# Kernel tuning notes

Hardware: AMD Instinct MI355X
Metric: run time of the kernel (lower is better)

## Reference

```python
import jax, jax.numpy as jnp
import numpy as np

EPSILON = 1e-05
LOG_2PI = float(np.log(2.0 * np.pi))


def setup_inputs() -> dict:
    key = jax.random.key(0)
    k1, k2, k3 = jax.random.split(key, 3)
    B, S, K, N = 64, 1000, 12, 80  # batch, seq, n_states, n_channels
    x = jax.random.normal(k1, (B, S, N), dtype=jnp.float32)
    mu = jax.random.normal(k2, (B, K, N), dtype=jnp.float32)
    # Positive-definite covariances per (batch, state)
    A = jax.random.normal(k3, (B, K, N, N), dtype=jnp.float32)
    sigma = A @ jnp.swapaxes(A, -1, -2) / N + jnp.eye(N, dtype=jnp.float32)
    return {"x": x, "mu": mu, "sigma": sigma}


def reference(x, mu, sigma):
    """Batched-over-states MVN log-likelihood.

    x: (B, S, N); mu: (B, K, N); sigma: (B, K, N, N).
    Returns log_likelihood: (B, S, K).
    """
    N = x.shape[-1]
    # add_epsilon with diag=True: epsilon * I on the diagonal
    sigma = sigma + jnp.asarray(EPSILON, sigma.dtype) * jnp.eye(N, dtype=sigma.dtype)
    L = jnp.linalg.cholesky(sigma)  # (B, K, N, N), batched across states
    diff = x[:, :, None, :] - mu[:, None, :, :]  # (B, S, K, N)
    # Solve L z = diff, batched: L -> (B, 1, K, N, N), diff -> (B, S, K, N, 1)
    z = jax.scipy.linalg.solve_triangular(L[:, None], diff[..., None], lower=True)[..., 0]
    quad = jnp.sum(z * z, axis=-1)  # (B, S, K)
    logdet_half = jnp.sum(jnp.log(jnp.diagonal(L, axis1=-2, axis2=-1)), axis=-1)  # (B, K)
    ll = -0.5 * quad - logdet_half[:, None, :] - 0.5 * N * jnp.asarray(LOG_2PI, x.dtype)
    return ll  # (B, S, K)
```

## Files before the change

kernel.cpp:

```cpp
#include <hip/hip_runtime.h>

#define Bb 64
#define Ss 1000
#define Kk 12
#define Nn 80
#define CTERM 73.51508265637381f
#define STA 84

typedef __attribute__((ext_vector_type(8))) short short8;
typedef __attribute__((ext_vector_type(4))) float f32x4;

static __device__ __forceinline__ unsigned short f2bf(float f) {
    unsigned u = __builtin_bit_cast(unsigned, f);
    unsigned r = u + 0x7FFFu + ((u >> 16) & 1u);
    return (unsigned short)(r >> 16);
}
static __device__ __forceinline__ float bf2f(unsigned short h) {
    unsigned u = ((unsigned)h) << 16;
    return __builtin_bit_cast(float, u);
}

__global__ __launch_bounds__(256, 3) void prep_kernel(
    const float* __restrict__ sigma, const float* __restrict__ mu,
    const float* __restrict__ x,
    uint4* __restrict__ wsWh, uint4* __restrict__ wsWl,
    float* __restrict__ wsV, float* __restrict__ wsL,
    uint4* __restrict__ Xh, uint4* __restrict__ Xl, int doX)
{
    __shared__ float Ls[Nn * STA];
    __shared__ float LT[Nn * Nn];
    __shared__ float invd[Nn];
    __shared__ float mus[Nn];
    __shared__ float ldp[4];

    const int bk  = blockIdx.x;
    const int tid = threadIdx.x;
    const int w   = tid >> 6;
    const int l   = tid & 63;
    const int r2  = l + 64;

    const float4* sp4 = (const float4*)(sigma + (size_t)bk * Nn * Nn);
    #pragma unroll
    for (int it = 0; it < 7; ++it) {
        int ci = tid + 256 * it;
        if (ci < 1600) {
            float4 v = sp4[ci];
            int r = ci / 20, c4 = 4 * (ci - 20 * r);
            *(float4*)&Ls[r * STA + c4] = v;
        }
    }
    if (tid < Nn) mus[tid] = mu[(size_t)bk * Nn + tid];
    __syncthreads();
    if (tid < Nn) Ls[tid * STA + tid] += 1e-5f;
    __syncthreads();

    float ldacc = 0.0f;
    for (int p = 0; p < 20; ++p) {
        const int j0 = 4 * p;
        const bool a1 = (l >= j0);
        const bool a2 = (l < 16) && (r2 >= j0);

        if (w == (p & 3)) {
            float B00 = Ls[j0*STA+j0];
            float B10 = Ls[(j0+1)*STA+j0], B11 = Ls[(j0+1)*STA+j0+1];
            float B20 = Ls[(j0+2)*STA+j0], B21 = Ls[(j0+2)*STA+j0+1], B22 = Ls[(j0+2)*STA+j0+2];
            float B30 = Ls[(j0+3)*STA+j0], B31 = Ls[(j0+3)*STA+j0+1], B32 = Ls[(j0+3)*STA+j0+2], B33 = Ls[(j0+3)*STA+j0+3];
            float rv0 = rsqrtf(B00);
            float l10 = B10*rv0, l20 = B20*rv0, l30 = B30*rv0;
            float t11 = fmaf(-l10,l10,B11);                    float rv1 = rsqrtf(t11);
            float l21 = fmaf(-l20,l10,B21)*rv1;
            float l31 = fmaf(-l30,l10,B31)*rv1;
            float t22 = fmaf(-l21,l21,fmaf(-l20,l20,B22));     float rv2 = rsqrtf(t22);
            float l32 = fmaf(-l31,l21,fmaf(-l30,l20,B32))*rv2;
            float t33 = fmaf(-l32,l32,fmaf(-l31,l31,fmaf(-l30,l30,B33)));
            float rv3 = rsqrtf(t33);
            ldacc += 0.5f * (logf(B00) + logf(t11) + logf(t22) + logf(t33));
            if (l == 0) { invd[j0]=rv0; invd[j0+1]=rv1; invd[j0+2]=rv2; invd[j0+3]=rv3; }

            float b0=0.f,b1=0.f,b2=0.f,b3=0.f, c0=0.f,c1=0.f,c2=0.f,c3=0.f;
            if (a1) {
                float4 a = *(float4*)&Ls[l * STA + j0];
                b0 = a.x * rv0;
                b1 = fmaf(-l10, b0, a.y) * rv1;
                b2 = fmaf(-l21, b1, fmaf(-l20, b0, a.z)) * rv2;
                b3 = fmaf(-l32, b2, fmaf(-l31, b1, fmaf(-l30, b0, a.w))) * rv3;
                *(float4*)&Ls[l * STA + j0] = make_float4(b0, b1, b2, b3);
            }
            if (a2) {
                float4 a = *(float4*)&Ls[r2 * STA + j0];
                c0 = a.x * rv0;
                c1 = fmaf(-l10, c0, a.y) * rv1;
                c2 = fmaf(-l21, c1, fmaf(-l20, c0, a.z)) * rv2;
                c3 = fmaf(-l32, c2, fmaf(-l31, c1, fmaf(-l30, c0, a.w))) * rv3;
                *(float4*)&Ls[r2 * STA + j0] = make_float4(c0, c1, c2, c3);
            }
            LT[ j0   *Nn + l] = (l  > j0  ) ? b0 : 0.f;
            LT[(j0+1)*Nn + l] = (l  > j0+1) ? b1 : 0.f;
            LT[(j0+2)*Nn + l] = (l  > j0+2) ? b2 : 0.f;
            LT[(j0+3)*Nn + l] = (l  > j0+3) ? b3 : 0.f;
            if (l < 16) {
                LT[ j0   *Nn + r2] = (r2 > j0  ) ? c0 : 0.f;
                LT[(j0+1)*Nn + r2] = (r2 > j0+1) ? c1 : 0.f;
                LT[(j0+2)*Nn + r2] = (r2 > j0+2) ? c2 : 0.f;
                LT[(j0+3)*Nn + r2] = (r2 > j0+3) ? c3 : 0.f;
            }
        }
        __syncthreads();

        float4 bv = make_float4(0.f,0.f,0.f,0.f), cv = make_float4(0.f,0.f,0.f,0.f);
        if (a1) bv = *(float4*)&Ls[l * STA + j0];
        if (a2) cv = *(float4*)&Ls[r2 * STA + j0];
        const int gs0 = p + 1;
        const int g0 = gs0 + ((w - gs0) & 3);
        #pragma unroll 2
        for (int g = g0; g < 20; g += 4) {
            float4 u0 = *(const float4*)&LT[ j0   *Nn + 4*g];
            float4 u1 = *(const float4*)&LT[(j0+1)*Nn + 4*g];
            float4 u2 = *(const float4*)&LT[(j0+2)*Nn + 4*g];
            float4 u3 = *(const float4*)&LT[(j0+3)*Nn + 4*g];
            if (a1) {
                float4 t = *(float4*)&Ls[l * STA + 4*g];
                t.x = fmaf(-bv.x,u0.x, fmaf(-bv.y,u1.x, fmaf(-bv.z,u2.x, fmaf(-bv.w,u3.x, t.x))));
                t.y = fmaf(-bv.x,u0.y, fmaf(-bv.y,u1.y, fmaf(-bv.z,u2.y, fmaf(-bv.w,u3.y, t.y))));
                t.z = fmaf(-bv.x,u0.z, fmaf(-bv.y,u1.z, fmaf(-bv.z,u2.z, fmaf(-bv.w,u3.z, t.z))));
                t.w = fmaf(-bv.x,u0.w, fmaf(-bv.y,u1.w, fmaf(-bv.z,u2.w, fmaf(-bv.w,u3.w, t.w))));
                *(float4*)&Ls[l * STA + 4*g] = t;
            }
            if (a2) {
                float4 t = *(float4*)&Ls[r2 * STA + 4*g];
                t.x = fmaf(-cv.x,u0.x, fmaf(-cv.y,u1.x, fmaf(-cv.z,u2.x, fmaf(-cv.w,u3.x, t.x))));
                t.y = fmaf(-cv.x,u0.y, fmaf(-cv.y,u1.y, fmaf(-cv.z,u2.y, fmaf(-cv.w,u3.y, t.y))));
                t.z = fmaf(-cv.x,u0.z, fmaf(-cv.y,u1.z, fmaf(-cv.z,u2.z, fmaf(-cv.w,u3.z, t.z))));
                t.w = fmaf(-cv.x,u0.w, fmaf(-cv.y,u1.w, fmaf(-cv.z,u2.w, fmaf(-cv.w,u3.w, t.w))));
                *(float4*)&Ls[r2 * STA + 4*g] = t;
            }
        }
    }
    if (l == 0) ldp[w] = ldacc;
    __syncthreads();
    if (tid == 0) wsL[bk] = ldp[0] + ldp[1] + ldp[2] + ldp[3];

    if (tid < Nn) {
        #pragma unroll
        for (int g = 0; g < 20; ++g)
            *(float4*)&Ls[tid * STA + 4*g] = make_float4(0.f, 0.f, 0.f, 0.f);
        Ls[tid * STA + tid] = 1.0f;
    }
    __syncthreads();

    for (int p = 0; p < 20; ++p) {
        const int i0 = 4 * p;
        const bool b1a = (i0 + 3 >= l);
        const bool b2a = (l < 16) && (i0 + 3 >= r2);

        if (w == (p & 3)) {
            float m10 = LT[ i0   *Nn + i0+1];
            float m20 = LT[ i0   *Nn + i0+2];
            float m30 = LT[ i0   *Nn + i0+3];
            float m21 = LT[(i0+1)*Nn + i0+2];
            float m31 = LT[(i0+1)*Nn + i0+3];
            float m32 = LT[(i0+2)*Nn + i0+3];
            float4 iv = *(const float4*)&invd[i0];
            if (b1a) {
                float4 a = *(float4*)&Ls[l * STA + i0];
                float w0 = a.x * iv.x;
                float w1 = fmaf(-w0, m10, a.y) * iv.y;
                float w2 = fmaf(-w1, m21, fmaf(-w0, m20, a.z)) * iv.z;
                float w3 = fmaf(-w2, m32, fmaf(-w1, m31, fmaf(-w0, m30, a.w))) * iv.w;
                *(float4*)&Ls[l * STA + i0] = make_float4(w0, w1, w2, w3);
            }
            if (b2a) {
                float4 a = *(float4*)&Ls[r2 * STA + i0];
                float v0 = a.x * iv.x;
                float v1 = fmaf(-v0, m10, a.y) * iv.y;
                float v2 = fmaf(-v1, m21, fmaf(-v0, m20, a.z)) * iv.z;
                float v3 = fmaf(-v2, m32, fmaf(-v1, m31, fmaf(-v0, m30, a.w))) * iv.w;
                *(float4*)&Ls[r2 * STA + i0] = make_float4(v0, v1, v2, v3);
            }
        }
        __syncthreads();

        float4 wv = make_float4(0.f,0.f,0.f,0.f), vv = make_float4(0.f,0.f,0.f,0.f);
        if (b1a) wv = *(float4*)&Ls[l * STA + i0];
        if (b2a) vv = *(float4*)&Ls[r2 * STA + i0];
        if (b1a | b2a) {
            const int gs0 = p + 1;
            const int g0 = gs0 + ((w - gs0) & 3);
            #pragma unroll 2
            for (int g = g0; g < 20; g += 4) {
                float4 u0 = *(const float4*)&LT[ i0   *Nn + 4*g];
                float4 u1 = *(const float4*)&LT[(i0+1)*Nn + 4*g];
                float4 u2 = *(const float4*)&LT[(i0+2)*Nn + 4*g];
                float4 u3 = *(const float4*)&LT[(i0+3)*Nn + 4*g];
                if (b1a) {
                    float4 t = *(float4*)&Ls[l * STA + 4*g];
                    t.x = fmaf(-wv.x,u0.x, fmaf(-wv.y,u1.x, fmaf(-wv.z,u2.x, fmaf(-wv.w,u3.x, t.x))));
                    t.y = fmaf(-wv.x,u0.y, fmaf(-wv.y,u1.y, fmaf(-wv.z,u2.y, fmaf(-wv.w,u3.y, t.y))));
                    t.z = fmaf(-wv.x,u0.z, fmaf(-wv.y,u1.z, fmaf(-wv.z,u2.z, fmaf(-wv.w,u3.z, t.z))));
                    t.w = fmaf(-wv.x,u0.w, fmaf(-wv.y,u1.w, fmaf(-wv.z,u2.w, fmaf(-wv.w,u3.w, t.w))));
                    *(float4*)&Ls[l * STA + 4*g] = t;
                }
                if (b2a) {
                    float4 t = *(float4*)&Ls[r2 * STA + 4*g];
                    t.x = fmaf(-vv.x,u0.x, fmaf(-vv.y,u1.x, fmaf(-vv.z,u2.x, fmaf(-vv.w,u3.x, t.x))));
                    t.y = fmaf(-vv.x,u0.y, fmaf(-vv.y,u1.y, fmaf(-vv.z,u2.y, fmaf(-vv.w,u3.y, t.y))));
                    t.z = fmaf(-vv.x,u0.z, fmaf(-vv.y,u1.z, fmaf(-vv.z,u2.z, fmaf(-vv.w,u3.z, t.z))));
                    t.w = fmaf(-vv.x,u0.w, fmaf(-vv.y,u1.w, fmaf(-vv.z,u2.w, fmaf(-vv.w,u3.w, t.w))));
                    *(float4*)&Ls[r2 * STA + 4*g] = t;
                }
            }
        }
    }
    __syncthreads();

    {
        float* vpart = LT;
        float s1 = 0.f, s2 = 0.f;
        const int c0 = 20 * w;
        #pragma unroll 4
        for (int cc = 0; cc < 20; ++cc) {
            int c = c0 + cc;
            float mc = mus[c];
            s1 = fmaf(Ls[c * STA + l], mc, s1);
            if (l < 16) s2 = fmaf(Ls[c * STA + r2], mc, s2);
        }
        vpart[w * Nn + l] = s1;
        if (l < 16) vpart[w * Nn + r2] = s2;
        __syncthreads();
        if (tid < Nn)
            wsV[(size_t)bk * Nn + tid] =
                vpart[tid] + vpart[Nn + tid] + vpart[2*Nn + tid] + vpart[3*Nn + tid];
    }
    const int n = l & 15, quad = l >> 4;
    uint4* ph = wsWh + (size_t)bk * 800;
    uint4* pq = wsWl + (size_t)bk * 800;
    for (int f = w; f < 10; f += 4) {
        int ks = f / 5, mt = f - 5 * ks;
        int m = 16 * mt + n, kb = 32 * ks + 8 * quad;
        unsigned hh[8], lo[8];
        #pragma unroll
        for (int j = 0; j < 8; ++j) {
            float wj = Ls[(kb + j) * STA + m];
            unsigned short h = f2bf(wj);
            hh[j] = h; lo[j] = f2bf(wj - bf2f(h));
        }
        ph[f*64 + l] = make_uint4(hh[0]|(hh[1]<<16), hh[2]|(hh[3]<<16), hh[4]|(hh[5]<<16), hh[6]|(hh[7]<<16));
        pq[f*64 + l] = make_uint4(lo[0]|(lo[1]<<16), lo[2]|(lo[3]<<16), lo[4]|(lo[5]<<16), lo[6]|(lo[7]<<16));
    }
    for (int mt = w; mt < 5; mt += 4) {
        if (quad < 2) {
            int m = 16 * mt + n, kb = 64 + 8 * quad;
            unsigned hh[8], lo[8];
            #pragma unroll
            for (int j = 0; j < 8; ++j) {
                float wj = Ls[(kb + j) * STA + m];
                unsigned short h = f2bf(wj);
                hh[j] = h; lo[j] = f2bf(wj - bf2f(h));
            }
            ph[640 + mt*32 + l] = make_uint4(hh[0]|(hh[1]<<16), hh[2]|(hh[3]<<16), hh[4]|(hh[5]<<16), hh[6]|(hh[7]<<16));
            pq[640 + mt*32 + l] = make_uint4(lo[0]|(lo[1]<<16), lo[2]|(lo[3]<<16), lo[4]|(lo[5]<<16), lo[6]|(lo[7]<<16));
        }
    }

    if (doX) {
        const int wid = bk * 4 + w;
        const int qd = l >> 4, n2 = l & 15;
        #pragma unroll
        for (int it = 0; it < 4; ++it) {
            int G = wid + 3072 * it;
            if (G >= 12096) break;
            int b2  = G / 189;
            int rem = G - b2 * 189;
            int sg  = rem / 3, ks = rem - 3 * sg;
            int s   = sg * 16 + n2;
            int k0  = 32 * ks + 8 * qd;
            float d[8] = {0.f,0.f,0.f,0.f,0.f,0.f,0.f,0.f};
            if (s < Ss) {
                const float* xp = x + ((size_t)b2 * Ss + s) * Nn + k0;
                float4 f0 = *(const float4*)xp;
                float4 f1 = *(const float4*)(xp + 4);
                d[0]=f0.x; d[1]=f0.y; d[2]=f0.z; d[3]=f0.w;
                d[4]=f1.x; d[5]=f1.y; d[6]=f1.z; d[7]=f1.w;
            }
            unsigned hh[8], lo[8];
            #pragma unroll
            for (int j = 0; j < 8; ++j) {
                unsigned short h = f2bf(d[j]);
                hh[j] = h; lo[j] = f2bf(d[j] - bf2f(h));
            }
            size_t slot = ((size_t)(b2 * 64 + sg) * 3 + ks) * 64 + l;
            Xh[slot] = make_uint4(hh[0]|(hh[1]<<16), hh[2]|(hh[3]<<16), hh[4]|(hh[5]<<16), hh[6]|(hh[7]<<16));
            Xl[slot] = make_uint4(lo[0]|(lo[1]<<16), lo[2]|(lo[3]<<16), lo[4]|(lo[5]<<16), lo[6]|(lo[7]<<16));
        }
    }
}

__global__ __launch_bounds__(256) void ll_kernel2(
    const uint4* __restrict__ Xh, const uint4* __restrict__ Xl,
    const uint4* __restrict__ wsWh, const uint4* __restrict__ wsWl,
    const float* __restrict__ wsV, const float* __restrict__ wsL,
    float* __restrict__ out)
{
    __shared__ uint4 WhL[960], WlL[960];
    const int b = blockIdx.x;
    const int k = blockIdx.y;
    const int bk = b * Kk + k;
    const int tid = threadIdx.x;
    const int wv = tid >> 6, lane = tid & 63;
    const int n = lane & 15, quad = lane >> 4;

    const uint4* gh = wsWh + (size_t)bk * 800;
    const uint4* gl = wsWl + (size_t)bk * 800;
    #pragma unroll
    for (int it = 0; it < 3; ++it) {
        int i = tid + 256 * it;
        if (i < 640) { WhL[i] = gh[i]; WlL[i] = gl[i]; }
    }
    #pragma unroll
    for (int it = 0; it < 2; ++it) {
        int i = tid + 256 * it;
        if (i < 320) {
            int mt = i >> 6, ln = i & 63, qd = (ln >> 4);
            uint4 vh = make_uint4(0,0,0,0), vl = make_uint4(0,0,0,0);
            if (qd < 2) { vh = gh[640 + mt*32 + ln]; vl = gl[640 + mt*32 + ln]; }
            WhL[640 + i] = vh; WlL[640 + i] = vl;
        }
    }
    __syncthreads();

    const float ld = wsL[bk];
    f32x4 vf[5];
    #pragma unroll
    for (int mt = 0; mt < 5; ++mt)
        vf[mt] = *(const f32x4*)&wsV[(size_t)bk * Nn + 16*mt + 4*quad];

    for (int st = 0; st < 8; ++st) {
        const int sg0 = st * 8 + wv * 2;
        short8 bh[2][3], bl[2][3];
        #pragma unroll
        for (int t = 0; t < 2; ++t)
            #pragma unroll
            for (int ks = 0; ks < 3; ++ks) {
                size_t base = ((size_t)(b * 64 + sg0 + t) * 3 + ks) * 64 + lane;
                bh[t][ks] = __builtin_bit_cast(short8, Xh[base]);
                bl[t][ks] = __builtin_bit_cast(short8, Xl[base]);
            }

        f32x4 acc[2][5];
        #pragma unroll
        for (int t = 0; t < 2; ++t)
            #pragma unroll
            for (int mt = 0; mt < 5; ++mt) acc[t][mt] = (f32x4){0.f,0.f,0.f,0.f};

        #pragma unroll
        for (int ks = 0; ks < 3; ++ks) {
            #pragma unroll
            for (int mt = 0; mt < 5; ++mt) {
                const int fi = (ks < 2) ? (ks*5 + mt)*64 + lane : 640 + mt*64 + lane;
                short8 wh = __builtin_bit_cast(short8, WhL[fi]);
                short8 wl = __builtin_bit_cast(short8, WlL[fi]);
                #pragma unroll
                for (int t = 0; t < 2; ++t) {
                    acc[t][mt] = __builtin_amdgcn_mfma_f32_16x16x32_bf16(wh, bh[t][ks], acc[t][mt], 0, 0, 0);
                    acc[t][mt] = __builtin_amdgcn_mfma_f32_16x16x32_bf16(wl, bh[t][ks], acc[t][mt], 0, 0, 0);
                    acc[t][mt] = __builtin_amdgcn_mfma_f32_16x16x32_bf16(wh, bl[t][ks], acc[t][mt], 0, 0, 0);
                }
            }
        }

        #pragma unroll
        for (int t = 0; t < 2; ++t) {
            float q2 = 0.f;
            #pragma unroll
            for (int mt = 0; mt < 5; ++mt)
                #pragma unroll
                for (int r = 0; r < 4; ++r) {
                    float y = acc[t][mt][r] - vf[mt][r];
                    q2 = fmaf(y, y, q2);
                }
            q2 += __shfl_xor(q2, 16, 64);
            q2 += __shfl_xor(q2, 32, 64);
            int gs = st * 128 + wv * 32 + 16 * t + n;
            if (lane < 16 && gs < Ss)
                out[((size_t)b * Ss + gs) * Kk + k] = -0.5f * q2 - ld - CTERM;
        }
    }
}

__global__ __launch_bounds__(256) void ll_kernel(
    const float* __restrict__ x,
    const uint4* __restrict__ wsWh, const uint4* __restrict__ wsWl,
    const float* __restrict__ wsV, const float* __restrict__ wsL,
    float* __restrict__ out)
{
    const int b    = blockIdx.x;
    const int st   = blockIdx.y;
    const int tid  = threadIdx.x;
    const int wv   = tid >> 6, lane = tid & 63;
    const int n    = lane & 15, quad = lane >> 4;
    const int sbase = st * 128 + wv * 32;

    short8 xh[2][3], xl[2][3];
    #pragma unroll
    for (int t = 0; t < 2; ++t) {
        int gs = sbase + 16 * t + n;
        #pragma unroll
        for (int ks = 0; ks < 3; ++ks) {
            int kb = 32 * ks + 8 * quad;
            float d[8] = {0.f,0.f,0.f,0.f,0.f,0.f,0.f,0.f};
            if (gs < Ss && kb < Nn) {
                const float* xp = x + ((size_t)b * Ss + gs) * Nn + kb;
                float4 f0 = *(const float4*)xp;
                float4 f1 = *(const float4*)(xp + 4);
                d[0]=f0.x; d[1]=f0.y; d[2]=f0.z; d[3]=f0.w;
                d[4]=f1.x; d[5]=f1.y; d[6]=f1.z; d[7]=f1.w;
            }
            short8 h, lo2;
            #pragma unroll
            for (int j = 0; j < 8; ++j) {
                unsigned short hv = f2bf(d[j]);
                h[j]   = (short)hv;
                lo2[j] = (short)f2bf(d[j] - bf2f(hv));
            }
            xh[t][ks] = h; xl[t][ks] = lo2;
        }
    }

    for (int k = 0; k < Kk; ++k) {
        const int bk = b * Kk + k;
        const uint4* ah_p = wsWh + (size_t)bk * 800;
        const uint4* al_p = wsWl + (size_t)bk * 800;

        f32x4 acc[2][5];
        #pragma unroll
        for (int t = 0; t < 2; ++t)
            #pragma unroll
            for (int mt = 0; mt < 5; ++mt) acc[t][mt] = (f32x4){0.f,0.f,0.f,0.f};

        #pragma unroll
        for (int ks = 0; ks < 3; ++ks) {
            short8 ah[5], al[5];
            if (ks < 2) {
                #pragma unroll
                for (int mt = 0; mt < 5; ++mt) {
                    ah[mt] = __builtin_bit_cast(short8, ah_p[(ks*5 + mt)*64 + lane]);
                    al[mt] = __builtin_bit_cast(short8, al_p[(ks*5 + mt)*64 + lane]);
                }
            } else {
                #pragma unroll
                for (int mt = 0; mt < 5; ++mt) {
                    uint4 zh = make_uint4(0,0,0,0), zl = make_uint4(0,0,0,0);
                    if (quad < 2) {
                        zh = ah_p[640 + mt*32 + lane];
                        zl = al_p[640 + mt*32 + lane];
                    }
                    ah[mt] = __builtin_bit_cast(short8, zh);
                    al[mt] = __builtin_bit_cast(short8, zl);
                }
            }
            #pragma unroll
            for (int mt = 0; mt < 5; ++mt)
                #pragma unroll
                for (int t = 0; t < 2; ++t) {
                    acc[t][mt] = __builtin_amdgcn_mfma_f32_16x16x32_bf16(ah[mt], xh[t][ks], acc[t][mt], 0, 0, 0);
                    acc[t][mt] = __builtin_amdgcn_mfma_f32_16x16x32_bf16(al[mt], xh[t][ks], acc[t][mt], 0, 0, 0);
                    acc[t][mt] = __builtin_amdgcn_mfma_f32_16x16x32_bf16(ah[mt], xl[t][ks], acc[t][mt], 0, 0, 0);
                }
        }

        float ld = wsL[bk];
        f32x4 vf[5];
        #pragma unroll
        for (int mt = 0; mt < 5; ++mt)
            vf[mt] = *(const f32x4*)&wsV[(size_t)bk * Nn + 16*mt + 4*quad];
        #pragma unroll
        for (int t = 0; t < 2; ++t) {
            float q2 = 0.f;
            #pragma unroll
            for (int mt = 0; mt < 5; ++mt)
                #pragma unroll
                for (int r = 0; r < 4; ++r) {
                    float y = acc[t][mt][r] - vf[mt][r];
                    q2 = fmaf(y, y, q2);
                }
            q2 += __shfl_xor(q2, 16, 64);
            q2 += __shfl_xor(q2, 32, 64);
            int gs = sbase + 16 * t + n;
            if (lane < 16 && gs < Ss)
                out[((size_t)b * Ss + gs) * Kk + k] = -0.5f * q2 - ld - CTERM;
        }
    }
}

#define ST1 81
__global__ __launch_bounds__(256) void mvn_ll_fallback(
    const float* __restrict__ x, const float* __restrict__ mu,
    const float* __restrict__ sigma, float* __restrict__ out)
{
    __shared__ float Ls[Nn * ST1];
    __shared__ float invd[Nn];
    __shared__ float mus[Nn];
    __shared__ float logdet_s;

    const int bk = blockIdx.x, b = bk / Kk, k = bk - b * Kk;
    const int tid = threadIdx.x, nt = blockDim.x;

    const float* sp = sigma + (size_t)bk * Nn * Nn;
    for (int t = tid; t < Nn * Nn; t += nt) Ls[(t / Nn) * ST1 + (t % Nn)] = sp[t];
    if (tid < Nn) mus[tid] = mu[(size_t)bk * Nn + tid];
    __syncthreads();
    if (tid < Nn) Ls[tid * ST1 + tid] += 1e-5f;
    __syncthreads();
    for (int j = 0; j < Nn; ++j) {
        if (tid == 0) {
            float d = sqrtf(Ls[j * ST1 + j]);
            Ls[j * ST1 + j] = d; invd[j] = 1.0f / d;
        }
        __syncthreads();
        const float inv = invd[j];
        for (int i = j + 1 + tid; i < Nn; i += nt) Ls[i * ST1 + j] *= inv;
        __syncthreads();
        for (int t = tid; t < Nn * Nn; t += nt) {
            int r = t / Nn, c = t % Nn;
            if (r > j && c > j && c <= r)
                Ls[r * ST1 + c] -= Ls[r * ST1 + j] * Ls[c * ST1 + j];
        }
        __syncthreads();
    }
    if (tid == 0) {
        float a = 0.f; for (int j = 0; j < Nn; ++j) a += logf(Ls[j * ST1 + j]);
        logdet_s = a;
    }
    __syncthreads();
    const float ld = logdet_s;
    for (int s = tid; s < Ss; s += nt) {
        const float4* xp = (const float4*)(x + ((size_t)b * Ss + s) * Nn);
        float a[Nn];
        #pragma unroll
        for (int q = 0; q < Nn / 4; ++q) {
            float4 v = xp[q];
            a[4*q+0] = v.x - mus[4*q+0]; a[4*q+1] = v.y - mus[4*q+1];
            a[4*q+2] = v.z - mus[4*q+2]; a[4*q+3] = v.w - mus[4*q+3];
        }
        #pragma unroll
        for (int i = 0; i < Nn; ++i) {
            float t = a[i];
            #pragma unroll
            for (int j = 0; j < i; ++j) t = fmaf(-Ls[i * ST1 + j], a[j], t);
            a[i] = t * invd[i];
        }
        float quad = 0.f;
        #pragma unroll
        for (int i = 0; i < Nn; ++i) quad = fmaf(a[i], a[i], quad);
        out[((size_t)b * Ss + s) * Kk + k] = -0.5f * quad - ld - CTERM;
    }
}

extern "C" void kernel_launch(void* const* d_in, const int* in_sizes, int n_in,
                              void* d_out, int out_size, void* d_ws, size_t ws_size,
                              hipStream_t stream) {
    const float* x     = (const float*)d_in[0];
    const float* mu    = (const float*)d_in[1];
    const float* sigma = (const float*)d_in[2];
    float* out = (float*)d_out;

    const size_t nBK   = (size_t)Bb * Kk;
    const size_t nWu4  = nBK * 800;
    const size_t nXu4  = (size_t)Bb * 64 * 3 * 64;
    const size_t need_mid  = nWu4 * 16 * 2 + nBK * Nn * 4 + nBK * 4;
    const size_t need_full = need_mid + nXu4 * 16 * 2;

    if (ws_size >= need_full) {
        uint4* wsWh = (uint4*)d_ws;
        uint4* wsWl = wsWh + nWu4;
        uint4* Xh   = wsWl + nWu4;
        uint4* Xl   = Xh + nXu4;
        float* wsV  = (float*)(Xl + nXu4);
        float* wsL  = wsV + nBK * Nn;
        prep_kernel<<<dim3(Bb * Kk), dim3(256), 0, stream>>>(
            sigma, mu, x, wsWh, wsWl, wsV, wsL, Xh, Xl, 1);
        ll_kernel2<<<dim3(Bb, Kk), dim3(256), 0, stream>>>(Xh, Xl, wsWh, wsWl, wsV, wsL, out);
    } else if (ws_size >= need_mid) {
        uint4* wsWh = (uint4*)d_ws;
        uint4* wsWl = wsWh + nWu4;
        float* wsV  = (float*)(wsWl + nWu4);
        float* wsL  = wsV + nBK * Nn;
        prep_kernel<<<dim3(Bb * Kk), dim3(256), 0, stream>>>(
            sigma, mu, x, wsWh, wsWl, wsV, wsL, (uint4*)nullptr, (uint4*)nullptr, 0);
        ll_kernel<<<dim3(Bb, 8), dim3(256), 0, stream>>>(x, wsWh, wsWl, wsV, wsL, out);
    } else {
        mvn_ll_fallback<<<dim3(Bb * Kk), dim3(256), 0, stream>>>(x, mu, sigma, out);
    }
}
```

Measured before the change: 168.1 us.

## Drop LT shared buffer, compute Cholesky and inverse in place in one array

Removes the separate transposed LT shared-memory array (about 25KB) so the factorization and the triangular inverse both run in place inside Ls. The trailing updates now read the panel columns straight from Ls, the identity is formed on the fly, and the lower triangle is masked when reading. The smaller shared footprint lets launch bounds rise from 3 to 5 blocks per CU for prep_kernel. In exchange the panel reads are now strided column reads from Ls, which may raise LDS bank conflicts, and extra masking logic is added.

```diff
diff --git a/kernel.cpp b/kernel.cpp
--- a/kernel.cpp
+++ b/kernel.cpp
@@ -20,7 +20,7 @@
     return __builtin_bit_cast(float, u);
 }
 
-__global__ __launch_bounds__(256, 3) void prep_kernel(
+__global__ __launch_bounds__(256, 5) void prep_kernel(
     const float* __restrict__ sigma, const float* __restrict__ mu,
     const float* __restrict__ x,
     uint4* __restrict__ wsWh, uint4* __restrict__ wsWl,
@@ -28,10 +28,10 @@
     uint4* __restrict__ Xh, uint4* __restrict__ Xl, int doX)
 {
     __shared__ float Ls[Nn * STA];
-    __shared__ float LT[Nn * Nn];
     __shared__ float invd[Nn];
     __shared__ float mus[Nn];
     __shared__ float ldp[4];
+    __shared__ float vps[4 * Nn];
 
     const int bk  = blockIdx.x;
     const int tid = threadIdx.x;
@@ -77,32 +77,21 @@
             ldacc += 0.5f * (logf(B00) + logf(t11) + logf(t22) + logf(t33));
             if (l == 0) { invd[j0]=rv0; invd[j0+1]=rv1; invd[j0+2]=rv2; invd[j0+3]=rv3; }
 
-            float b0=0.f,b1=0.f,b2=0.f,b3=0.f, c0=0.f,c1=0.f,c2=0.f,c3=0.f;
             if (a1) {
                 float4 a = *(float4*)&Ls[l * STA + j0];
-                b0 = a.x * rv0;
-                b1 = fmaf(-l10, b0, a.y) * rv1;
-                b2 = fmaf(-l21, b1, fmaf(-l20, b0, a.z)) * rv2;
-                b3 = fmaf(-l32, b2, fmaf(-l31, b1, fmaf(-l30, b0, a.w))) * rv3;
+                float b0 = a.x * rv0;
+                float b1 = fmaf(-l10, b0, a.y) * rv1;
+                float b2 = fmaf(-l21, b1, fmaf(-l20, b0, a.z)) * rv2;
+                float b3 = fmaf(-l32, b2, fmaf(-l31, b1, fmaf(-l30, b0, a.w))) * rv3;
                 *(float4*)&Ls[l * STA + j0] = make_float4(b0, b1, b2, b3);
             }
             if (a2) {
                 float4 a = *(float4*)&Ls[r2 * STA + j0];
-                c0 = a.x * rv0;
-                c1 = fmaf(-l10, c0, a.y) * rv1;
-                c2 = fmaf(-l21, c1, fmaf(-l20, c0, a.z)) * rv2;
-                c3 = fmaf(-l32, c2, fmaf(-l31, c1, fmaf(-l30, c0, a.w))) * rv3;
+                float c0 = a.x * rv0;
+                float c1 = fmaf(-l10, c0, a.y) * rv1;
+                float c2 = fmaf(-l21, c1, fmaf(-l20, c0, a.z)) * rv2;
+                float c3 = fmaf(-l32, c2, fmaf(-l31, c1, fmaf(-l30, c0, a.w))) * rv3;
                 *(float4*)&Ls[r2 * STA + j0] = make_float4(c0, c1, c2, c3);
-            }
-            LT[ j0   *Nn + l] = (l  > j0  ) ? b0 : 0.f;
-            LT[(j0+1)*Nn + l] = (l  > j0+1) ? b1 : 0.f;
-            LT[(j0+2)*Nn + l] = (l  > j0+2) ? b2 : 0.f;
-            LT[(j0+3)*Nn + l] = (l  > j0+3) ? b3 : 0.f;
-            if (l < 16) {
-                LT[ j0   *Nn + r2] = (r2 > j0  ) ? c0 : 0.f;
-                LT[(j0+1)*Nn + r2] = (r2 > j0+1) ? c1 : 0.f;
-                LT[(j0+2)*Nn + r2] = (r2 > j0+2) ? c2 : 0.f;
-                LT[(j0+3)*Nn + r2] = (r2 > j0+3) ? c3 : 0.f;
             }
         }
         __syncthreads();
@@ -114,24 +103,24 @@
         const int g0 = gs0 + ((w - gs0) & 3);
         #pragma unroll 2
         for (int g = g0; g < 20; g += 4) {
-            float4 u0 = *(const float4*)&LT[ j0   *Nn + 4*g];
-            float4 u1 = *(const float4*)&LT[(j0+1)*Nn + 4*g];
-            float4 u2 = *(const float4*)&LT[(j0+2)*Nn + 4*g];
-            float4 u3 = *(const float4*)&LT[(j0+3)*Nn + 4*g];
+            float4 q0 = *(const float4*)&Ls[(4*g+0) * STA + j0];
+            float4 q1 = *(const float4*)&Ls[(4*g+1) * STA + j0];
+            float4 q2 = *(const float4*)&Ls[(4*g+2) * STA + j0];
+            float4 q3 = *(const float4*)&Ls[(4*g+3) * STA + j0];
             if (a1) {
                 float4 t = *(float4*)&Ls[l * STA + 4*g];
-                t.x = fmaf(-bv.x,u0.x, fmaf(-bv.y,u1.x, fmaf(-bv.z,u2.x, fmaf(-bv.w,u3.x, t.x))));
-                t.y = fmaf(-bv.x,u0.y, fmaf(-bv.y,u1.y, fmaf(-bv.z,u2.y, fmaf(-bv.w,u3.y, t.y))));
-                t.z = fmaf(-bv.x,u0.z, fmaf(-bv.y,u1.z, fmaf(-bv.z,u2.z, fmaf(-bv.w,u3.z, t.z))));
-                t.w = fmaf(-bv.x,u0.w, fmaf(-bv.y,u1.w, fmaf(-bv.z,u2.w, fmaf(-bv.w,u3.w, t.w))));
+                t.x = fmaf(-bv.x,q0.x, fmaf(-bv.y,q0.y, fmaf(-bv.z,q0.z, fmaf(-bv.w,q0.w, t.x))));
+                t.y = fmaf(-bv.x,q1.x, fmaf(-bv.y,q1.y, fmaf(-bv.z,q1.z, fmaf(-bv.w,q1.w, t.y))));
+                t.z = fmaf(-bv.x,q2.x, fmaf(-bv.y,q2.y, fmaf(-bv.z,q2.z, fmaf(-bv.w,q2.w, t.z))));
+                t.w = fmaf(-bv.x,q3.x, fmaf(-bv.y,q3.y, fmaf(-bv.z,q3.z, fmaf(-bv.w,q3.w, t.w))));
                 *(float4*)&Ls[l * STA + 4*g] = t;
             }
             if (a2) {
                 float4 t = *(float4*)&Ls[r2 * STA + 4*g];
-                t.x = fmaf(-cv.x,u0.x, fmaf(-cv.y,u1.x, fmaf(-cv.z,u2.x, fmaf(-cv.w,u3.x, t.x))));
-                t.y = fmaf(-cv.x,u0.y, fmaf(-cv.y,u1.y, fmaf(-cv.z,u2.y, fmaf(-cv.w,u3.y, t.y))));
-                t.z = fmaf(-cv.x,u0.z, fmaf(-cv.y,u1.z, fmaf(-cv.z,u2.z, fmaf(-cv.w,u3.z, t.z))));
-                t.w = fmaf(-cv.x,u0.w, fmaf(-cv.y,u1.w, fmaf(-cv.z,u2.w, fmaf(-cv.w,u3.w, t.w))));
+                t.x = fmaf(-cv.x,q0.x, fmaf(-cv.y,q0.y, fmaf(-cv.z,q0.z, fmaf(-cv.w,q0.w, t.x))));
+                t.y = fmaf(-cv.x,q1.x, fmaf(-cv.y,q1.y, fmaf(-cv.z,q1.z, fmaf(-cv.w,q1.w, t.y))));
+                t.z = fmaf(-cv.x,q2.x, fmaf(-cv.y,q2.y, fmaf(-cv.z,q2.z, fmaf(-cv.w,q2.w, t.z))));
+                t.w = fmaf(-cv.x,q3.x, fmaf(-cv.y,q3.y, fmaf(-cv.z,q3.z, fmaf(-cv.w,q3.w, t.w))));
                 *(float4*)&Ls[r2 * STA + 4*g] = t;
             }
         }
@@ -140,11 +129,9 @@
     __syncthreads();
     if (tid == 0) wsL[bk] = ldp[0] + ldp[1] + ldp[2] + ldp[3];
 
-    if (tid < Nn) {
-        #pragma unroll
-        for (int g = 0; g < 20; ++g)
-            *(float4*)&Ls[tid * STA + 4*g] = make_float4(0.f, 0.f, 0.f, 0.f);
-        Ls[tid * STA + tid] = 1.0f;
+    for (int i = tid; i < Nn * Nn; i += 256) {
+        int r = i / Nn, c = i - Nn * r;
+        if (c > r) Ls[r * STA + c] = 0.0f;
     }
     __syncthreads();
 
@@ -154,15 +141,17 @@
         const bool b2a = (l < 16) && (i0 + 3 >= r2);
 
         if (w == (p & 3)) {
-            float m10 = LT[ i0   *Nn + i0+1];
-            float m20 = LT[ i0   *Nn + i0+2];
-            float m30 = LT[ i0   *Nn + i0+3];
-            float m21 = LT[(i0+1)*Nn + i0+2];
-            float m31 = LT[(i0+1)*Nn + i0+3];
-            float m32 = LT[(i0+2)*Nn + i0+3];
+            float m10 = Ls[(i0+1)*STA + i0];
+            float m20 = Ls[(i0+2)*STA + i0];
+            float m30 = Ls[(i0+3)*STA + i0];
+            float m21 = Ls[(i0+2)*STA + i0+1];
+            float m31 = Ls[(i0+3)*STA + i0+1];
+            float m32 = Ls[(i0+3)*STA + i0+2];
             float4 iv = *(const float4*)&invd[i0];
             if (b1a) {
                 float4 a = *(float4*)&Ls[l * STA + i0];
+                if (l >= i0)
+                    a = make_float4(l==i0?1.f:0.f, l==i0+1?1.f:0.f, l==i0+2?1.f:0.f, l==i0+3?1.f:0.f);
                 float w0 = a.x * iv.x;
                 float w1 = fmaf(-w0, m10, a.y) * iv.y;
                 float w2 = fmaf(-w1, m21, fmaf(-w0, m20, a.z)) * iv.z;
@@ -171,6 +160,8 @@
             }
             if (b2a) {
                 float4 a = *(float4*)&Ls[r2 * STA + i0];
+                if (r2 >= i0)
+                    a = make_float4(r2==i0?1.f:0.f, r2==i0+1?1.f:0.f, r2==i0+2?1.f:0.f, r2==i0+3?1.f:0.f);
                 float v0 = a.x * iv.x;
                 float v1 = fmaf(-v0, m10, a.y) * iv.y;
                 float v2 = fmaf(-v1, m21, fmaf(-v0, m20, a.z)) * iv.z;
@@ -188,24 +179,24 @@
             const int g0 = gs0 + ((w - gs0) & 3);
             #pragma unroll 2
             for (int g = g0; g < 20; g += 4) {
-                float4 u0 = *(const float4*)&LT[ i0   *Nn + 4*g];
-                float4 u1 = *(const float4*)&LT[(i0+1)*Nn + 4*g];
-                float4 u2 = *(const float4*)&LT[(i0+2)*Nn + 4*g];
-                float4 u3 = *(const float4*)&LT[(i0+3)*Nn + 4*g];
+                float4 q0 = *(const float4*)&Ls[(4*g+0) * STA + i0];
+                float4 q1 = *(const float4*)&Ls[(4*g+1) * STA + i0];
+                float4 q2 = *(const float4*)&Ls[(4*g+2) * STA + i0];
+                float4 q3 = *(const float4*)&Ls[(4*g+3) * STA + i0];
                 if (b1a) {
                     float4 t = *(float4*)&Ls[l * STA + 4*g];
-                    t.x = fmaf(-wv.x,u0.x, fmaf(-wv.y,u1.x, fmaf(-wv.z,u2.x, fmaf(-wv.w,u3.x, t.x))));
-                    t.y = fmaf(-wv.x,u0.y, fmaf(-wv.y,u1.y, fmaf(-wv.z,u2.y, fmaf(-wv.w,u3.y, t.y))));
-                    t.z = fmaf(-wv.x,u0.z, fmaf(-wv.y,u1.z, fmaf(-wv.z,u2.z, fmaf(-wv.w,u3.z, t.z))));
-                    t.w = fmaf(-wv.x,u0.w, fmaf(-wv.y,u1.w, fmaf(-wv.z,u2.w, fmaf(-wv.w,u3.w, t.w))));
+                    t.x = fmaf(-wv.x,q0.x, fmaf(-wv.y,q0.y, fmaf(-wv.z,q0.z, fmaf(-wv.w,q0.w, t.x))));
+                    t.y = fmaf(-wv.x,q1.x, fmaf(-wv.y,q1.y, fmaf(-wv.z,q1.z, fmaf(-wv.w,q1.w, t.y))));
+                    t.z = fmaf(-wv.x,q2.x, fmaf(-wv.y,q2.y, fmaf(-wv.z,q2.z, fmaf(-wv.w,q2.w, t.z))));
+                    t.w = fmaf(-wv.x,q3.x, fmaf(-wv.y,q3.y, fmaf(-wv.z,q3.z, fmaf(-wv.w,q3.w, t.w))));
                     *(float4*)&Ls[l * STA + 4*g] = t;
                 }
                 if (b2a) {
                     float4 t = *(float4*)&Ls[r2 * STA + 4*g];
-                    t.x = fmaf(-vv.x,u0.x, fmaf(-vv.y,u1.x, fmaf(-vv.z,u2.x, fmaf(-vv.w,u3.x, t.x))));
-                    t.y = fmaf(-vv.x,u0.y, fmaf(-vv.y,u1.y, fmaf(-vv.z,u2.y, fmaf(-vv.w,u3.y, t.y))));
-                    t.z = fmaf(-vv.x,u0.z, fmaf(-vv.y,u1.z, fmaf(-vv.z,u2.z, fmaf(-vv.w,u3.z, t.z))));
-                    t.w = fmaf(-vv.x,u0.w, fmaf(-vv.y,u1.w, fmaf(-vv.z,u2.w, fmaf(-vv.w,u3.w, t.w))));
+                    t.x = fmaf(-vv.x,q0.x, fmaf(-vv.y,q0.y, fmaf(-vv.z,q0.z, fmaf(-vv.w,q0.w, t.x))));
+                    t.y = fmaf(-vv.x,q1.x, fmaf(-vv.y,q1.y, fmaf(-vv.z,q1.z, fmaf(-vv.w,q1.w, t.y))));
+                    t.z = fmaf(-vv.x,q2.x, fmaf(-vv.y,q2.y, fmaf(-vv.z,q2.z, fmaf(-vv.w,q2.w, t.z))));
+                    t.w = fmaf(-vv.x,q3.x, fmaf(-vv.y,q3.y, fmaf(-vv.z,q3.z, fmaf(-vv.w,q3.w, t.w))));
                     *(float4*)&Ls[r2 * STA + 4*g] = t;
                 }
             }
@@ -214,23 +205,27 @@
     __syncthreads();
 
     {
-        float* vpart = LT;
         float s1 = 0.f, s2 = 0.f;
         const int c0 = 20 * w;
         #pragma unroll 4
         for (int cc = 0; cc < 20; ++cc) {
             int c = c0 + cc;
             float mc = mus[c];
-            s1 = fmaf(Ls[c * STA + l], mc, s1);
-            if (l < 16) s2 = fmaf(Ls[c * STA + r2], mc, s2);
-        }
-        vpart[w * Nn + l] = s1;
-        if (l < 16) vpart[w * Nn + r2] = s2;
+            float e1 = (c <= l)  ? Ls[c * STA + l]  : 0.f;
+            s1 = fmaf(e1, mc, s1);
+            if (l < 16) {
+                float e2 = (c <= r2) ? Ls[c * STA + r2] : 0.f;
+                s2 = fmaf(e2, mc, s2);
+            }
+        }
+        vps[w * Nn + l] = s1;
+        if (l < 16) vps[w * Nn + r2] = s2;
         __syncthreads();
         if (tid < Nn)
             wsV[(size_t)bk * Nn + tid] =
-                vpart[tid] + vpart[Nn + tid] + vpart[2*Nn + tid] + vpart[3*Nn + tid];
-    }
+                vps[tid] + vps[Nn + tid] + vps[2*Nn + tid] + vps[3*Nn + tid];
+    }
+
     const int n = l & 15, quad = l >> 4;
     uint4* ph = wsWh + (size_t)bk * 800;
     uint4* pq = wsWl + (size_t)bk * 800;
@@ -240,7 +235,7 @@
         unsigned hh[8], lo[8];
         #pragma unroll
         for (int j = 0; j < 8; ++j) {
-            float wj = Ls[(kb + j) * STA + m];
+            float wj = (m >= kb + j) ? Ls[(kb + j) * STA + m] : 0.f;
             unsigned short h = f2bf(wj);
             hh[j] = h; lo[j] = f2bf(wj - bf2f(h));
         }
@@ -253,7 +248,7 @@
             unsigned hh[8], lo[8];
             #pragma unroll
             for (int j = 0; j < 8; ++j) {
-                float wj = Ls[(kb + j) * STA + m];
+                float wj = (m >= kb + j) ? Ls[(kb + j) * STA + m] : 0.f;
                 unsigned short h = f2bf(wj);
                 hh[j] = h; lo[j] = f2bf(wj - bf2f(h));
             }
```

Result: no change. 169.7 us (+0.9%).
